# Kernel optimization log

Hardware: AMD Instinct MI355X
Metric: run time of the kernel (lower is better)

The kernel has to match this reference:

```python
import jax, jax.numpy as jnp
import numpy as np

N, E = 50000, 500000
HID, H, D = 128, 8, 16
ED, EGD = 32, 64


def _ln(x, g, b):
    m = x.mean(-1, keepdims=True)
    v = ((x - m) ** 2).mean(-1, keepdims=True)
    return (x - m) / jnp.sqrt(v + 1e-5) * g + b


def _gelu(x):
    return jax.nn.gelu(x, approximate=False)  # torch nn.GELU default (erf)


def setup_inputs() -> dict:
    key = jax.random.key(0)
    ks = jax.random.split(key, 24)
    s = lambda k, shape, scale=0.05: jax.random.normal(k, shape, jnp.float32) * scale
    inp = {
        "x": jax.random.normal(ks[0], (N, HID), jnp.float32),
        "edge_attr": jax.random.normal(ks[1], (E, ED), jnp.float32),
        "gamma": jax.random.uniform(ks[2], (N, HID), jnp.float32),
        "beta": jax.random.normal(ks[3], (N, HID), jnp.float32) * 0.1,
        "Wq": s(ks[4], (HID, H * D)),
        "Wk": s(ks[5], (HID, H * D)),
        "Wv": s(ks[6], (HID, H * D)),
        "Wo": s(ks[7], (H * D, HID)),
        "bo": jnp.zeros((HID,), jnp.float32),
        "ea_w1": s(ks[8], (ED, EGD)), "ea_b1": jnp.zeros((EGD,), jnp.float32),
        "ea_w2": s(ks[9], (EGD, H)), "ea_b2": jnp.zeros((H,), jnp.float32),
        "eg_w1": s(ks[10], (ED, EGD)), "eg_b1": jnp.zeros((EGD,), jnp.float32),
        "eg_w2": s(ks[11], (EGD, H * D)), "eg_b2": jnp.zeros((H * D,), jnp.float32),
        "ln1_g": jnp.ones((HID,), jnp.float32), "ln1_b": jnp.zeros((HID,), jnp.float32),
        "ln2_g": jnp.ones((HID,), jnp.float32), "ln2_b": jnp.zeros((HID,), jnp.float32),
        "ffn_w1": s(ks[12], (HID, 2 * HID)), "ffn_b1": jnp.zeros((2 * HID,), jnp.float32),
        "ffn_w2": s(ks[13], (2 * HID, HID)), "ffn_b2": jnp.zeros((HID,), jnp.float32),
        "edge_index": jax.random.randint(ks[14], (2, E), 0, N, jnp.int32),
    }
    return inp


def reference(x, edge_attr, gamma, beta, Wq, Wk, Wv, Wo, bo,
              ea_w1, ea_b1, ea_w2, ea_b2, eg_w1, eg_b1, eg_w2, eg_b2,
              ln1_g, ln1_b, ln2_g, ln2_b, ffn_w1, ffn_b1, ffn_w2, ffn_b2,
              edge_index):
    n = x.shape[0]
    src, dst = edge_index[0], edge_index[1]
    xn = _ln(x, ln1_g, ln1_b)
    Q = (xn @ Wq).reshape(n, H, D)
    K = (xn @ Wk).reshape(n, H, D)
    V = (xn @ Wv).reshape(n, H, D)
    # per-edge attention logits [E, H]
    logits = (Q[dst] * K[src]).sum(-1) * (D ** -0.5)
    logits = logits + (_gelu(edge_attr @ ea_w1 + ea_b1) @ ea_w2 + ea_b2)
    # sparse softmax over edges sharing a destination; torch version
    # initializes max buffer to zeros (include_self), so clamp max at 0
    m = jnp.maximum(jax.ops.segment_max(logits, dst, num_segments=n), 0.0)
    ex = jnp.exp(logits - m[dst])
    ssum = jax.ops.segment_sum(ex, dst, num_segments=n)
    attn = ex / (ssum[dst] + 1e-10)
    gate = jax.nn.sigmoid(_gelu(edge_attr @ eg_w1 + eg_b1) @ eg_w2 + eg_b2).reshape(-1, H, D)
    weighted = attn[..., None] * (gate * V[src])  # [E, H, D]
    agg = jax.ops.segment_sum(weighted, dst, num_segments=n).reshape(n, H * D)
    out = agg @ Wo + bo
    out = gamma * out + beta
    x = x + out
    x2 = _ln(x, ln2_g, ln2_b)
    f = _gelu(x2 @ ffn_w1 + ffn_b1) @ ffn_w2 + ffn_b2
    return x + f
```

## Files before the change

kernel.cpp:

```cpp
#include <hip/hip_runtime.h>

constexpr int N   = 50000;
constexpr int E   = 500000;
constexpr int HID = 128;
constexpr int NH  = 8;
constexpr int ED  = 32;
constexpr int EGD = 64;
constexpr int NB  = (N + 255) / 256;

typedef short  bf16x8 __attribute__((ext_vector_type(8)));
typedef float  f32x4  __attribute__((ext_vector_type(4)));

__device__ __forceinline__ float gelu_f(float v) {
    float u = v * v;
    float a = v * fmaf(u, -0.07135481283f, -1.5957691216f);
    float e = __expf(a);
    return v * __builtin_amdgcn_rcpf(1.f + e);
}
__device__ __forceinline__ float sigm_f(float v) {
    float e = __expf(-v);
    return __builtin_amdgcn_rcpf(1.f + e);
}
__device__ __forceinline__ unsigned short f2bf(float f) {
    return __builtin_bit_cast(unsigned short, static_cast<__bf16>(f));
}
__device__ __forceinline__ unsigned int pk2bf(float lo, float hi) {
    return (unsigned int)f2bf(lo) | ((unsigned int)f2bf(hi) << 16);
}
__device__ __forceinline__ float dot2(unsigned int a, unsigned int b) {
    float al = __uint_as_float(a << 16), ah = __uint_as_float(a & 0xffff0000u);
    float bl = __uint_as_float(b << 16), bh = __uint_as_float(b & 0xffff0000u);
    return al * bl + ah * bh;
}

__global__ __launch_bounds__(256) void k_cvt(
    const float* __restrict__ Wq, const float* __restrict__ Wk,
    const float* __restrict__ Wv, const float* __restrict__ Wo,
    const float* __restrict__ fw1, const float* __restrict__ fw2,
    const float* __restrict__ ea_w1, const float* __restrict__ ea_w2,
    const float* __restrict__ eg_w1, const float* __restrict__ eg_w2,
    unsigned short* __restrict__ dst)
{
    int f = blockIdx.x * 256 + threadIdx.x;
    if (f >= 18048) return;
    const float* W; int KT, srcN, base;
    if      (f < 2048)  { W = Wq;    KT = 4; srcN = 128; base = 0; }
    else if (f < 4096)  { W = Wk;    KT = 4; srcN = 128; base = 2048; }
    else if (f < 6144)  { W = Wv;    KT = 4; srcN = 128; base = 4096; }
    else if (f < 8192)  { W = Wo;    KT = 4; srcN = 128; base = 6144; }
    else if (f < 12288) { W = fw1;   KT = 4; srcN = 256; base = 8192; }
    else if (f < 16384) { W = fw2;   KT = 8; srcN = 128; base = 12288; }
    else if (f < 16640) { W = ea_w1; KT = 1; srcN = 64;  base = 16384; }
    else if (f < 16768) { W = ea_w2; KT = 2; srcN = 8;   base = 16640; }
    else if (f < 17024) { W = eg_w1; KT = 1; srcN = 64;  base = 16768; }
    else                { W = eg_w2; KT = 2; srcN = 128; base = 17024; }
    int fl = f - base, lane = fl & 63, t = fl >> 6;
    int ks = t % KT, nt = t / KT;
    int n  = nt * 16 + (lane & 15);
    int k0 = ks * 32 + (lane >> 4) * 8;
    union { unsigned short u[8]; uint4 v; } o;
#pragma unroll
    for (int j = 0; j < 8; j++)
        o.u[j] = (n < srcN) ? f2bf(W[(size_t)(k0 + j) * srcN + n]) : (unsigned short)0;
    *(uint4*)(dst + (size_t)f * 8) = o.v;
}

__global__ __launch_bounds__(256) void k_ln_qkv_mfma(
    const float* __restrict__ x, const float* __restrict__ g1, const float* __restrict__ b1,
    const unsigned short* __restrict__ wqkv,
    unsigned short* __restrict__ Q, unsigned short* __restrict__ K, unsigned short* __restrict__ V)
{
    __shared__ unsigned short xn_lds[16 * 128];
    const int tid = threadIdx.x;
    const int nodeBase = blockIdx.x * 16;

    {
        int nl = tid >> 4, q = tid & 15;
        const float4* xp = (const float4*)(x + (size_t)(nodeBase + nl) * HID + q * 8);
        float4 t0 = xp[0], t1 = xp[1];
        float v[8] = {t0.x, t0.y, t0.z, t0.w, t1.x, t1.y, t1.z, t1.w};
        float s = 0.f, ss = 0.f;
#pragma unroll
        for (int i = 0; i < 8; i++) { s += v[i]; ss += v[i] * v[i]; }
        s += __shfl_xor(s, 1); ss += __shfl_xor(ss, 1);
        s += __shfl_xor(s, 2); ss += __shfl_xor(ss, 2);
        s += __shfl_xor(s, 4); ss += __shfl_xor(ss, 4);
        s += __shfl_xor(s, 8); ss += __shfl_xor(ss, 8);
        float mean = s * (1.f / HID);
        float ri = rsqrtf(ss * (1.f / HID) - mean * mean + 1e-5f);
        union { unsigned short u[8]; uint4 v4; } o;
#pragma unroll
        for (int c = 0; c < 8; c++) {
            int col = q * 8 + c;
            o.u[c] = f2bf((v[c] - mean) * ri * g1[col] + b1[col]);
        }
        *(uint4*)&xn_lds[nl * 128 + (q ^ nl) * 8] = o.v4;
    }
    __syncthreads();

    const int wv = tid >> 6, lane = tid & 63;
    const int lm = lane & 15, kb = lane >> 4, rowq = kb * 4;
    bf16x8 af[4];
#pragma unroll
    for (int ks = 0; ks < 4; ks++)
        af[ks] = *(const bf16x8*)&xn_lds[lm * 128 + ((ks * 4 + kb) ^ lm) * 8];

    const int node = nodeBase + lm;
#pragma unroll
    for (int u = 0; u < 6; u++) {
        int nt = 6 * wv + u;
        f32x4 c = {0.f, 0.f, 0.f, 0.f};
#pragma unroll
        for (int ks = 0; ks < 4; ks++)
            c = __builtin_amdgcn_mfma_f32_16x16x32_bf16(
                    *(const bf16x8*)&wqkv[((size_t)(nt * 4 + ks) * 64 + lane) * 8],
                    af[ks], c, 0, 0, 0);
        unsigned short* O = (nt < 8) ? Q : ((nt < 16) ? K : V);
        uint2 o = make_uint2(pk2bf(c[0], c[1]), pk2bf(c[2], c[3]));
        *(uint2*)(O + (size_t)node * HID + (nt & 7) * 16 + rowq) = o;
    }
}

__global__ __launch_bounds__(256) void k_hist(const int* __restrict__ ei, int* __restrict__ cnt) {
    int e = blockIdx.x * 256 + threadIdx.x;
    if (e < E) atomicAdd(&cnt[ei[E + e]], 1);
}

__global__ __launch_bounds__(256) void k_bsum(const int* __restrict__ cnt, int* __restrict__ bsum) {
    int i = blockIdx.x * 256 + threadIdx.x;
    int v = (i < N) ? cnt[i] : 0;
#pragma unroll
    for (int m = 1; m < 64; m <<= 1) v += __shfl_xor(v, m);
    __shared__ int ws4[4];
    if ((threadIdx.x & 63) == 0) ws4[threadIdx.x >> 6] = v;
    __syncthreads();
    if (threadIdx.x == 0) bsum[blockIdx.x] = ws4[0] + ws4[1] + ws4[2] + ws4[3];
}

__global__ __launch_bounds__(256) void k_scan_b(const int* __restrict__ bsum, int* __restrict__ boff) {
    __shared__ int s[256];
    int t = threadIdx.x;
    int v = (t < NB) ? bsum[t] : 0;
    s[t] = v; __syncthreads();
    for (int off = 1; off < 256; off <<= 1) {
        int add = (t >= off) ? s[t - off] : 0;
        __syncthreads();
        s[t] += add;
        __syncthreads();
    }
    if (t < NB) boff[t] = s[t] - v;
}

__global__ __launch_bounds__(256) void k_scan_final(
    const int* __restrict__ cnt, const int* __restrict__ boff,
    int* __restrict__ starts, int* __restrict__ cursor)
{
    __shared__ int s[256];
    int t = threadIdx.x, i = blockIdx.x * 256 + t;
    int v = (i < N) ? cnt[i] : 0;
    s[t] = v; __syncthreads();
    for (int off = 1; off < 256; off <<= 1) {
        int add = (t >= off) ? s[t - off] : 0;
        __syncthreads();
        s[t] += add;
        __syncthreads();
    }
    int ex = boff[blockIdx.x] + s[t] - v;
    if (i < N) {
        starts[i] = ex;
        cursor[i] = ex;
        if (i == N - 1) starts[N] = ex + v;
    }
}

__global__ __launch_bounds__(256) void k_scatter(
    const int* __restrict__ ei, int* __restrict__ cursor, uint4* __restrict__ esd)
{
    int e = blockIdx.x * 256 + threadIdx.x;
    if (e < E) {
        int src = ei[e], dst = ei[E + e];
        int p = atomicAdd(&cursor[dst], 1);
        esd[p] = make_uint4((unsigned)src, (unsigned)dst, (unsigned)e, 0u);
    }
}

__global__ __launch_bounds__(256) void k_edge(
    const float* __restrict__ edge_attr, const uint4* __restrict__ esd,
    const unsigned short* __restrict__ Qb, const unsigned short* __restrict__ Kb,
    const unsigned short* __restrict__ Vb,
    const unsigned short* __restrict__ w1ea, const float* __restrict__ b1ea,
    const unsigned short* __restrict__ w2ea, const float* __restrict__ b2ea,
    const unsigned short* __restrict__ w1eg, const float* __restrict__ b1eg,
    const unsigned short* __restrict__ w2eg, const float* __restrict__ b2eg,
    float* __restrict__ logit_s, unsigned int* __restrict__ gv)
{
    __shared__ unsigned short ea_lds[256 * 32];
    __shared__ unsigned short sc_lds[4 * 16 * 64];
    __shared__ int perm_lds[256];
    __shared__ int src_lds[256];
    float* st16 = (float*)ea_lds;

    const int tid   = threadIdx.x;
    const int jBase = blockIdx.x * 256;
    const int lane  = tid & 63;
    const int wv    = tid >> 6;
    const int wBase = wv * 64;
    const int lm    = lane & 15;
    const int kb    = lane >> 4;
    const int rowq  = kb * 4;

    const int j  = jBase + tid;
    const int jj = (j < E) ? j : E - 1;
    const uint4 r4 = esd[jj];
    {
        perm_lds[tid] = (int)r4.z;
        src_lds[tid]  = (int)r4.x;
    }
    __syncthreads();

#pragma unroll
    for (int it = 0; it < 8; it++) {
        int idx = it * 256 + tid;
        int el = idx >> 3, c = (idx & 7) * 4;
        int ge = perm_lds[el];
        float4 v = *(const float4*)(edge_attr + (size_t)ge * ED + c);
        int g = ((c >> 3) ^ (el & 3));
        *(uint2*)&ea_lds[el * 32 + g * 8 + (c & 7)] =
            make_uint2(pk2bf(v.x, v.y), pk2bf(v.z, v.w));
    }
    __syncthreads();

    unsigned short* sc = &sc_lds[wv * 1024];

#pragma unroll 1
    for (int et = 0; et < 4; et++) {
        const int am = wBase + et * 16 + lm;
        const bf16x8 a1 = *(const bf16x8*)&ea_lds[am * 32 + (kb ^ (am & 3)) * 8];

        {
            f32x4 acc[4];
#pragma unroll
            for (int nt = 0; nt < 4; nt++) {
                f32x4 z = {0.f, 0.f, 0.f, 0.f};
                acc[nt] = __builtin_amdgcn_mfma_f32_16x16x32_bf16(
                    a1, *(const bf16x8*)&w1ea[(nt * 64 + lane) * 8], z, 0, 0, 0);
            }
#pragma unroll
            for (int nt = 0; nt < 4; nt++) {
                float bias = b1ea[nt * 16 + lm];
#pragma unroll
                for (int r = 0; r < 4; r++) {
                    int el = rowq + r;
                    int kg = nt * 2 + (lm >> 3);
                    sc[el * 64 + ((kg ^ (el & 7)) * 8) + (lm & 7)] =
                        f2bf(gelu_f(acc[nt][r] + bias));
                }
            }
        }
        {
            bf16x8 f0 = *(const bf16x8*)&sc[lm * 64 + ((kb ^ (lm & 7)) * 8)];
            bf16x8 f1 = *(const bf16x8*)&sc[lm * 64 + (((4 + kb) ^ (lm & 7)) * 8)];
            float bias = b2ea[lm & 7];
            f32x4 acc = {bias, bias, bias, bias};
            acc = __builtin_amdgcn_mfma_f32_16x16x32_bf16(
                f0, *(const bf16x8*)&w2ea[(0 * 64 + lane) * 8], acc, 0, 0, 0);
            acc = __builtin_amdgcn_mfma_f32_16x16x32_bf16(
                f1, *(const bf16x8*)&w2ea[(1 * 64 + lane) * 8], acc, 0, 0, 0);
            if (lm < 8) {
#pragma unroll
                for (int r = 0; r < 4; r++)
                    st16[(wBase + et * 16 + rowq + r) * 16 + lm] = acc[r];
            }
        }
        {
            f32x4 acc[4];
#pragma unroll
            for (int nt = 0; nt < 4; nt++) {
                f32x4 z = {0.f, 0.f, 0.f, 0.f};
                acc[nt] = __builtin_amdgcn_mfma_f32_16x16x32_bf16(
                    a1, *(const bf16x8*)&w1eg[(nt * 64 + lane) * 8], z, 0, 0, 0);
            }
#pragma unroll
            for (int nt = 0; nt < 4; nt++) {
                float bias = b1eg[nt * 16 + lm];
#pragma unroll
                for (int r = 0; r < 4; r++) {
                    int el = rowq + r;
                    int kg = nt * 2 + (lm >> 3);
                    sc[el * 64 + ((kg ^ (el & 7)) * 8) + (lm & 7)] =
                        f2bf(gelu_f(acc[nt][r] + bias));
                }
            }
        }
        {
            bf16x8 h0 = *(const bf16x8*)&sc[lm * 64 + ((kb ^ (lm & 7)) * 8)];
            bf16x8 h1 = *(const bf16x8*)&sc[lm * 64 + (((4 + kb) ^ (lm & 7)) * 8)];
            const int e   = jBase + wBase + et * 16 + lm;
            const int src = src_lds[wBase + et * 16 + lm];
            const unsigned short* vrow = Vb + (size_t)src * HID;
            const bool ok = (e < E);
            unsigned int* gvo = gv + (size_t)e * 64 + kb * 2;
#pragma unroll
            for (int mt = 0; mt < 8; mt++) {
                float4 b4 = *(const float4*)&b2eg[mt * 16 + rowq];
                f32x4 acc = {b4.x, b4.y, b4.z, b4.w};
                acc = __builtin_amdgcn_mfma_f32_16x16x32_bf16(
                    *(const bf16x8*)&w2eg[((mt * 2 + 0) * 64 + lane) * 8], h0, acc, 0, 0, 0);
                acc = __builtin_amdgcn_mfma_f32_16x16x32_bf16(
                    *(const bf16x8*)&w2eg[((mt * 2 + 1) * 64 + lane) * 8], h1, acc, 0, 0, 0);
                uint2 vv = *(const uint2*)(vrow + mt * 16 + rowq);
                float w0 = sigm_f(acc[0]) * __uint_as_float(vv.x << 16);
                float w1 = sigm_f(acc[1]) * __uint_as_float(vv.x & 0xffff0000u);
                float w2 = sigm_f(acc[2]) * __uint_as_float(vv.y << 16);
                float w3 = sigm_f(acc[3]) * __uint_as_float(vv.y & 0xffff0000u);
                uint2 o = make_uint2(pk2bf(w0, w1), pk2bf(w2, w3));
                if (ok) *(uint2*)(gvo + mt * 8) = o;
            }
        }
    }

    {
        if (j < E) {
            int src = (int)r4.x, dst = (int)r4.y;
            const uint4* qp = (const uint4*)(Qb + (size_t)dst * HID);
            const uint4* kp = (const uint4*)(Kb + (size_t)src * HID);
            float lg[8];
#pragma unroll
            for (int h = 0; h < 8; h++) {
                float dot = 0.f;
#pragma unroll
                for (int t = 0; t < 2; t++) {
                    uint4 q = qp[h * 2 + t], k4 = kp[h * 2 + t];
                    dot += dot2(q.x, k4.x) + dot2(q.y, k4.y) + dot2(q.z, k4.z) + dot2(q.w, k4.w);
                }
                lg[h] = __expf(fminf(st16[tid * 16 + h] + 0.25f * dot, 80.f));
            }
            float4* op = (float4*)(logit_s + (size_t)j * NH);
            op[0] = make_float4(lg[0], lg[1], lg[2], lg[3]);
            op[1] = make_float4(lg[4], lg[5], lg[6], lg[7]);
        }
    }
}

__global__ __launch_bounds__(256) void k_agg2(
    const int* __restrict__ starts, const unsigned int* __restrict__ gv,
    const float* __restrict__ logit_s, float* __restrict__ agg)
{
    int wave = threadIdx.x >> 6, lane = threadIdx.x & 63;
    int dst = blockIdx.x * 4 + wave;
    if (dst >= N) return;
    int s0 = starts[dst], s1 = starts[dst + 1];
    int head = lane >> 3;
    float ssum = 0.f, ax = 0.f, ay = 0.f;
#pragma unroll 4
    for (int j = s0; j < s1; j++) {
        float e = logit_s[(size_t)j * NH + head];
        unsigned int u = gv[(size_t)j * 64 + lane];
        ssum += e;
        ax += e * __uint_as_float(u << 16);
        ay += e * __uint_as_float(u & 0xffff0000u);
    }
    float rs = __builtin_amdgcn_rcpf(ssum + 1e-10f);
    float2* o = (float2*)(agg + (size_t)dst * HID + lane * 2);
    *o = make_float2(ax * rs, ay * rs);
}

__global__ __launch_bounds__(256) void k_node_out_mfma(
    const float* __restrict__ x, const float* __restrict__ gamma, const float* __restrict__ beta,
    const unsigned short* __restrict__ wo_f, const float* __restrict__ bo,
    const float* __restrict__ g2, const float* __restrict__ b2,
    const unsigned short* __restrict__ fw1_f, const float* __restrict__ fb1,
    const unsigned short* __restrict__ fw2_f, const float* __restrict__ fb2,
    const float* __restrict__ agg, float* __restrict__ out)
{
    __shared__ unsigned short a_lds[16 * 128];
    __shared__ unsigned short f1_lds[16 * 256];
    __shared__ float2 sums_lds[16][4];
    const int tid = threadIdx.x;
    const int nodeBase = blockIdx.x * 16;

    {
        int nl = tid >> 4, q = tid & 15;
        const float4* ap = (const float4*)(agg + (size_t)(nodeBase + nl) * HID + q * 8);
        float4 t0 = ap[0], t1 = ap[1];
        uint4 o = make_uint4(pk2bf(t0.x, t0.y), pk2bf(t0.z, t0.w),
                             pk2bf(t1.x, t1.y), pk2bf(t1.z, t1.w));
        *(uint4*)&a_lds[nl * 128 + (q ^ nl) * 8] = o;
    }
    __syncthreads();

    const int wv = tid >> 6, lane = tid & 63;
    const int lm = lane & 15, kb = lane >> 4, rowq = kb * 4;

    f32x4 xo[2];
    {
        bf16x8 af[4];
#pragma unroll
        for (int ks = 0; ks < 4; ks++)
            af[ks] = *(const bf16x8*)&a_lds[lm * 128 + ((ks * 4 + kb) ^ lm) * 8];
#pragma unroll
        for (int t = 0; t < 2; t++) {
            int nt = 2 * wv + t;
            f32x4 c = {0.f, 0.f, 0.f, 0.f};
#pragma unroll
            for (int ks = 0; ks < 4; ks++)
                c = __builtin_amdgcn_mfma_f32_16x16x32_bf16(
                        af[ks], *(const bf16x8*)&wo_f[((size_t)(nt * 4 + ks) * 64 + lane) * 8],
                        c, 0, 0, 0);
            xo[t] = c;
        }
    }

    float x1v[2][4];
#pragma unroll
    for (int t = 0; t < 2; t++) {
        int col = (2 * wv + t) * 16 + lm;
        float boc = bo[col];
#pragma unroll
        for (int r = 0; r < 4; r++) {
            size_t idx = (size_t)(nodeBase + rowq + r) * HID + col;
            x1v[t][r] = x[idx] + gamma[idx] * (xo[t][r] + boc) + beta[idx];
        }
    }

    {
        float s2[4], q2[4];
#pragma unroll
        for (int r = 0; r < 4; r++) {
            s2[r] = x1v[0][r] + x1v[1][r];
            q2[r] = x1v[0][r] * x1v[0][r] + x1v[1][r] * x1v[1][r];
        }
#pragma unroll
        for (int m = 1; m < 16; m <<= 1)
#pragma unroll
            for (int r = 0; r < 4; r++) { s2[r] += __shfl_xor(s2[r], m); q2[r] += __shfl_xor(q2[r], m); }
        if (lm == 0) {
#pragma unroll
            for (int r = 0; r < 4; r++)
                sums_lds[rowq + r][wv] = make_float2(s2[r], q2[r]);
        }
    }
    __syncthreads();
    float mu4[4], ri4[4];
#pragma unroll
    for (int r = 0; r < 4; r++) {
        float2 p0 = sums_lds[rowq + r][0], p1 = sums_lds[rowq + r][1];
        float2 p2 = sums_lds[rowq + r][2], p3 = sums_lds[rowq + r][3];
        float s = p0.x + p1.x + p2.x + p3.x;
        float q = p0.y + p1.y + p2.y + p3.y;
        float mu = s * (1.f / HID);
        mu4[r] = mu;
        ri4[r] = rsqrtf(q * (1.f / HID) - mu * mu + 1e-5f);
    }

#pragma unroll
    for (int t = 0; t < 2; t++) {
        int col = (2 * wv + t) * 16 + lm;
        float g2c = g2[col], b2c = b2[col];
#pragma unroll
        for (int r = 0; r < 4; r++) {
            float xn = (x1v[t][r] - mu4[r]) * ri4[r] * g2c + b2c;
            int row = rowq + r;
            int g = col >> 3;
            a_lds[row * 128 + (g ^ row) * 8 + (col & 7)] = f2bf(xn);
        }
    }
    __syncthreads();

    {
        bf16x8 af[4];
#pragma unroll
        for (int ks = 0; ks < 4; ks++)
            af[ks] = *(const bf16x8*)&a_lds[lm * 128 + ((ks * 4 + kb) ^ lm) * 8];
#pragma unroll
        for (int u = 0; u < 4; u++) {
            int nt = 4 * wv + u;
            f32x4 c = {0.f, 0.f, 0.f, 0.f};
#pragma unroll
            for (int ks = 0; ks < 4; ks++)
                c = __builtin_amdgcn_mfma_f32_16x16x32_bf16(
                        af[ks], *(const bf16x8*)&fw1_f[((size_t)(nt * 4 + ks) * 64 + lane) * 8],
                        c, 0, 0, 0);
            int col = nt * 16 + lm;
            float fbc = fb1[col];
#pragma unroll
            for (int r = 0; r < 4; r++) {
                int row = rowq + r;
                int g = col >> 3;
                int phys = (g & 16) | ((g ^ row) & 15);
                f1_lds[row * 256 + phys * 8 + (col & 7)] = f2bf(gelu_f(c[r] + fbc));
            }
        }
    }
    __syncthreads();

    {
        bf16x8 af[8];
#pragma unroll
        for (int ks = 0; ks < 8; ks++) {
            int g = ks * 4 + kb;
            int phys = (g & 16) | ((g ^ lm) & 15);
            af[ks] = *(const bf16x8*)&f1_lds[lm * 256 + phys * 8];
        }
#pragma unroll
        for (int t = 0; t < 2; t++) {
            int nt = 2 * wv + t;
            f32x4 c = {0.f, 0.f, 0.f, 0.f};
#pragma unroll
            for (int ks = 0; ks < 8; ks++)
                c = __builtin_amdgcn_mfma_f32_16x16x32_bf16(
                        af[ks], *(const bf16x8*)&fw2_f[((size_t)(nt * 8 + ks) * 64 + lane) * 8],
                        c, 0, 0, 0);
            int col = nt * 16 + lm;
            float fbc = fb2[col];
#pragma unroll
            for (int r = 0; r < 4; r++) {
                int node = nodeBase + rowq + r;
                out[(size_t)node * HID + col] = x1v[t][r] + c[r] + fbc;
            }
        }
    }
}

extern "C" void kernel_launch(void* const* d_in, const int* in_sizes, int n_in,
                              void* d_out, int out_size, void* d_ws, size_t ws_size,
                              hipStream_t stream)
{
    const float* x         = (const float*)d_in[0];
    const float* edge_attr = (const float*)d_in[1];
    const float* gamma     = (const float*)d_in[2];
    const float* beta      = (const float*)d_in[3];
    const float* Wq        = (const float*)d_in[4];
    const float* Wk        = (const float*)d_in[5];
    const float* Wv        = (const float*)d_in[6];
    const float* Wo        = (const float*)d_in[7];
    const float* bo        = (const float*)d_in[8];
    const float* ea_w1     = (const float*)d_in[9];
    const float* ea_b1     = (const float*)d_in[10];
    const float* ea_w2     = (const float*)d_in[11];
    const float* ea_b2     = (const float*)d_in[12];
    const float* eg_w1     = (const float*)d_in[13];
    const float* eg_b1     = (const float*)d_in[14];
    const float* eg_w2     = (const float*)d_in[15];
    const float* eg_b2     = (const float*)d_in[16];
    const float* ln1_g     = (const float*)d_in[17];
    const float* ln1_b     = (const float*)d_in[18];
    const float* ln2_g     = (const float*)d_in[19];
    const float* ln2_b     = (const float*)d_in[20];
    const float* fw1       = (const float*)d_in[21];
    const float* fb1       = (const float*)d_in[22];
    const float* fw2       = (const float*)d_in[23];
    const float* fb2       = (const float*)d_in[24];
    const int*   ei        = (const int*)d_in[25];

    char* wsb = (char*)d_ws;
    size_t off = 0;
    auto alloc = [&](size_t bytes) { void* p = wsb + off; off += (bytes + 255) & ~(size_t)255; return p; };

    unsigned short* Qb = (unsigned short*)alloc((size_t)N * HID * 2);
    unsigned short* Kb = (unsigned short*)alloc((size_t)N * HID * 2);
    unsigned short* Vb = (unsigned short*)alloc((size_t)N * HID * 2);
    float* logit_s = (float*)alloc((size_t)E * NH * 4);
    float* aggb    = (float*)alloc((size_t)N * HID * 4);
    int*   cnt     = (int*)alloc((size_t)N * 4);
    int*   starts  = (int*)alloc((size_t)(N + 1) * 4);
    int*   cursor  = (int*)alloc((size_t)N * 4);
    int*   bsum    = (int*)alloc((size_t)NB * 4);
    int*   boff    = (int*)alloc((size_t)NB * 4);
    uint4* esd     = (uint4*)alloc((size_t)E * 16);
    unsigned int*   gvb   = (unsigned int*)alloc((size_t)E * 64 * 4);
    unsigned short* fragW = (unsigned short*)alloc((size_t)18048 * 8 * 2);
    float* outp = (float*)d_out;

    unsigned short* wqkv_f = fragW;
    unsigned short* wo_f   = fragW + (size_t)6144  * 8;
    unsigned short* fw1_f  = fragW + (size_t)8192  * 8;
    unsigned short* fw2_f  = fragW + (size_t)12288 * 8;
    unsigned short* w1ea_f = fragW + (size_t)16384 * 8;
    unsigned short* w2ea_f = fragW + (size_t)16640 * 8;
    unsigned short* w1eg_f = fragW + (size_t)16768 * 8;
    unsigned short* w2eg_f = fragW + (size_t)17024 * 8;

    hipMemsetAsync(cnt, 0, (size_t)N * sizeof(int), stream);

    const int EB = (E + 255) / 256;
    const int NBLK16 = (N + 15) / 16;
    k_cvt<<<(18048 + 255) / 256, 256, 0, stream>>>(Wq, Wk, Wv, Wo, fw1, fw2,
                                                   ea_w1, ea_w2, eg_w1, eg_w2, fragW);
    k_ln_qkv_mfma<<<NBLK16, 256, 0, stream>>>(x, ln1_g, ln1_b, wqkv_f, Qb, Kb, Vb);
    k_hist<<<EB, 256, 0, stream>>>(ei, cnt);
    k_bsum<<<NB, 256, 0, stream>>>(cnt, bsum);
    k_scan_b<<<1, 256, 0, stream>>>(bsum, boff);
    k_scan_final<<<NB, 256, 0, stream>>>(cnt, boff, starts, cursor);
    k_scatter<<<EB, 256, 0, stream>>>(ei, cursor, esd);
    k_edge<<<EB, 256, 0, stream>>>(edge_attr, esd, Qb, Kb, Vb,
                                   w1ea_f, ea_b1, w2ea_f, ea_b2,
                                   w1eg_f, eg_b1, w2eg_f, eg_b2,
                                   logit_s, gvb);
    k_agg2<<<(N + 3) / 4, 256, 0, stream>>>(starts, gvb, logit_s, aggb);
    k_node_out_mfma<<<NBLK16, 256, 0, stream>>>(x, gamma, beta, wo_f, bo, ln2_g, ln2_b,
                                                fw1_f, fb1, fw2_f, fb2, aggb, outp);
}
```

Measured before the change: 446.1 us.

## Fuse preprocessing kernels and fold edge aggregation into node output kernel

```diff
diff --git a/kernel.cpp b/kernel.cpp
--- a/kernel.cpp
+++ b/kernel.cpp
@@ -7,6 +7,8 @@
 constexpr int ED  = 32;
 constexpr int EGD = 64;
 constexpr int NB  = (N + 255) / 256;
+constexpr int EB  = (E + 255) / 256;
+constexpr int NBLK16 = (N + 15) / 16;
 
 typedef short  bf16x8 __attribute__((ext_vector_type(8)));
 typedef float  f32x4  __attribute__((ext_vector_type(4)));
@@ -33,7 +35,8 @@
     return al * bl + ah * bh;
 }
 
-__global__ __launch_bounds__(256) void k_cvt(
+__global__ __launch_bounds__(256) void k_hist_cvt(
+    const int* __restrict__ ei, int* __restrict__ cnt,
     const float* __restrict__ Wq, const float* __restrict__ Wk,
     const float* __restrict__ Wv, const float* __restrict__ Wo,
     const float* __restrict__ fw1, const float* __restrict__ fw2,
@@ -41,7 +44,12 @@
     const float* __restrict__ eg_w1, const float* __restrict__ eg_w2,
     unsigned short* __restrict__ dst)
 {
-    int f = blockIdx.x * 256 + threadIdx.x;
+    if (blockIdx.x < EB) {
+        int e = blockIdx.x * 256 + threadIdx.x;
+        if (e < E) atomicAdd(&cnt[ei[E + e]], 1);
+        return;
+    }
+    int f = (blockIdx.x - EB) * 256 + threadIdx.x;
     if (f >= 18048) return;
     const float* W; int KT, srcN, base;
     if      (f < 2048)  { W = Wq;    KT = 4; srcN = 128; base = 0; }
@@ -65,13 +73,28 @@
     *(uint4*)(dst + (size_t)f * 8) = o.v;
 }
 
-__global__ __launch_bounds__(256) void k_ln_qkv_mfma(
+__global__ __launch_bounds__(256) void k_lnqkv_bsum(
     const float* __restrict__ x, const float* __restrict__ g1, const float* __restrict__ b1,
     const unsigned short* __restrict__ wqkv,
-    unsigned short* __restrict__ Q, unsigned short* __restrict__ K, unsigned short* __restrict__ V)
+    unsigned short* __restrict__ Q, unsigned short* __restrict__ K, unsigned short* __restrict__ V,
+    const int* __restrict__ cnt, int* __restrict__ bsum)
 {
     __shared__ unsigned short xn_lds[16 * 128];
     const int tid = threadIdx.x;
+
+    if (blockIdx.x >= NBLK16) {
+        int bb = blockIdx.x - NBLK16;
+        int i = bb * 256 + tid;
+        int v = (i < N) ? cnt[i] : 0;
+#pragma unroll
+        for (int m = 1; m < 64; m <<= 1) v += __shfl_xor(v, m);
+        int* ws4 = (int*)xn_lds;
+        if ((tid & 63) == 0) ws4[tid >> 6] = v;
+        __syncthreads();
+        if (tid == 0) bsum[bb] = ws4[0] + ws4[1] + ws4[2] + ws4[3];
+        return;
+    }
+
     const int nodeBase = blockIdx.x * 16;
 
     {
@@ -121,42 +144,22 @@
     }
 }
 
-__global__ __launch_bounds__(256) void k_hist(const int* __restrict__ ei, int* __restrict__ cnt) {
-    int e = blockIdx.x * 256 + threadIdx.x;
-    if (e < E) atomicAdd(&cnt[ei[E + e]], 1);
-}
-
-__global__ __launch_bounds__(256) void k_bsum(const int* __restrict__ cnt, int* __restrict__ bsum) {
-    int i = blockIdx.x * 256 + threadIdx.x;
-    int v = (i < N) ? cnt[i] : 0;
-#pragma unroll
-    for (int m = 1; m < 64; m <<= 1) v += __shfl_xor(v, m);
+__global__ __launch_bounds__(256) void k_scan_final2(
+    const int* __restrict__ cnt, const int* __restrict__ bsum,
+    int* __restrict__ starts, int* __restrict__ cursor)
+{
+    __shared__ int s[256];
     __shared__ int ws4[4];
-    if ((threadIdx.x & 63) == 0) ws4[threadIdx.x >> 6] = v;
-    __syncthreads();
-    if (threadIdx.x == 0) bsum[blockIdx.x] = ws4[0] + ws4[1] + ws4[2] + ws4[3];
-}
-
-__global__ __launch_bounds__(256) void k_scan_b(const int* __restrict__ bsum, int* __restrict__ boff) {
-    __shared__ int s[256];
-    int t = threadIdx.x;
-    int v = (t < NB) ? bsum[t] : 0;
-    s[t] = v; __syncthreads();
-    for (int off = 1; off < 256; off <<= 1) {
-        int add = (t >= off) ? s[t - off] : 0;
-        __syncthreads();
-        s[t] += add;
-        __syncthreads();
-    }
-    if (t < NB) boff[t] = s[t] - v;
-}
-
-__global__ __launch_bounds__(256) void k_scan_final(
-    const int* __restrict__ cnt, const int* __restrict__ boff,
-    int* __restrict__ starts, int* __restrict__ cursor)
-{
-    __shared__ int s[256];
-    int t = threadIdx.x, i = blockIdx.x * 256 + t;
+    const int t = threadIdx.x, b = blockIdx.x;
+
+    int pv = (t < b) ? bsum[t] : 0;
+#pragma unroll
+    for (int m = 1; m < 64; m <<= 1) pv += __shfl_xor(pv, m);
+    if ((t & 63) == 0) ws4[t >> 6] = pv;
+    __syncthreads();
+    const int pre = ws4[0] + ws4[1] + ws4[2] + ws4[3];
+
+    int i = b * 256 + t;
     int v = (i < N) ? cnt[i] : 0;
     s[t] = v; __syncthreads();
     for (int off = 1; off < 256; off <<= 1) {
@@ -165,7 +168,7 @@
         s[t] += add;
         __syncthreads();
     }
-    int ex = boff[blockIdx.x] + s[t] - v;
+    int ex = pre + s[t] - v;
     if (i < N) {
         starts[i] = ex;
         cursor[i] = ex;
@@ -342,36 +345,14 @@
     }
 }
 
-__global__ __launch_bounds__(256) void k_agg2(
-    const int* __restrict__ starts, const unsigned int* __restrict__ gv,
-    const float* __restrict__ logit_s, float* __restrict__ agg)
-{
-    int wave = threadIdx.x >> 6, lane = threadIdx.x & 63;
-    int dst = blockIdx.x * 4 + wave;
-    if (dst >= N) return;
-    int s0 = starts[dst], s1 = starts[dst + 1];
-    int head = lane >> 3;
-    float ssum = 0.f, ax = 0.f, ay = 0.f;
-#pragma unroll 4
-    for (int j = s0; j < s1; j++) {
-        float e = logit_s[(size_t)j * NH + head];
-        unsigned int u = gv[(size_t)j * 64 + lane];
-        ssum += e;
-        ax += e * __uint_as_float(u << 16);
-        ay += e * __uint_as_float(u & 0xffff0000u);
-    }
-    float rs = __builtin_amdgcn_rcpf(ssum + 1e-10f);
-    float2* o = (float2*)(agg + (size_t)dst * HID + lane * 2);
-    *o = make_float2(ax * rs, ay * rs);
-}
-
 __global__ __launch_bounds__(256) void k_node_out_mfma(
     const float* __restrict__ x, const float* __restrict__ gamma, const float* __restrict__ beta,
     const unsigned short* __restrict__ wo_f, const float* __restrict__ bo,
     const float* __restrict__ g2, const float* __restrict__ b2,
     const unsigned short* __restrict__ fw1_f, const float* __restrict__ fb1,
     const unsigned short* __restrict__ fw2_f, const float* __restrict__ fb2,
-    const float* __restrict__ agg, float* __restrict__ out)
+    const int* __restrict__ starts, const unsigned int* __restrict__ gv,
+    const float* __restrict__ logit_s, float* __restrict__ out)
 {
     __shared__ unsigned short a_lds[16 * 128];
     __shared__ unsigned short f1_lds[16 * 256];
@@ -379,18 +360,30 @@
     const int tid = threadIdx.x;
     const int nodeBase = blockIdx.x * 16;
 
-    {
-        int nl = tid >> 4, q = tid & 15;
-        const float4* ap = (const float4*)(agg + (size_t)(nodeBase + nl) * HID + q * 8);
-        float4 t0 = ap[0], t1 = ap[1];
-        uint4 o = make_uint4(pk2bf(t0.x, t0.y), pk2bf(t0.z, t0.w),
-                             pk2bf(t1.x, t1.y), pk2bf(t1.z, t1.w));
-        *(uint4*)&a_lds[nl * 128 + (q ^ nl) * 8] = o;
-    }
-    __syncthreads();
-
     const int wv = tid >> 6, lane = tid & 63;
     const int lm = lane & 15, kb = lane >> 4, rowq = kb * 4;
+
+#pragma unroll 1
+    for (int i = 0; i < 4; i++) {
+        const int nl = wv * 4 + i;
+        const int dst = nodeBase + nl;
+        const int s0 = starts[dst], s1 = starts[dst + 1];
+        const int head = lane >> 3;
+        float ssum = 0.f, ax = 0.f, ay = 0.f;
+#pragma unroll 4
+        for (int jj = s0; jj < s1; jj++) {
+            float e = logit_s[(size_t)jj * NH + head];
+            unsigned int u = gv[(size_t)jj * 64 + lane];
+            ssum += e;
+            ax += e * __uint_as_float(u << 16);
+            ay += e * __uint_as_float(u & 0xffff0000u);
+        }
+        float rs = __builtin_amdgcn_rcpf(ssum + 1e-10f);
+        int g = lane >> 2;
+        *(unsigned int*)&a_lds[nl * 128 + ((g ^ nl) * 8) + ((2 * lane) & 7)] =
+            pk2bf(ax * rs, ay * rs);
+    }
+    __syncthreads();
 
     f32x4 xo[2];
     {
@@ -561,12 +554,10 @@
     unsigned short* Kb = (unsigned short*)alloc((size_t)N * HID * 2);
     unsigned short* Vb = (unsigned short*)alloc((size_t)N * HID * 2);
     float* logit_s = (float*)alloc((size_t)E * NH * 4);
-    float* aggb    = (float*)alloc((size_t)N * HID * 4);
     int*   cnt     = (int*)alloc((size_t)N * 4);
     int*   starts  = (int*)alloc((size_t)(N + 1) * 4);
     int*   cursor  = (int*)alloc((size_t)N * 4);
     int*   bsum    = (int*)alloc((size_t)NB * 4);
-    int*   boff    = (int*)alloc((size_t)NB * 4);
     uint4* esd     = (uint4*)alloc((size_t)E * 16);
     unsigned int*   gvb   = (unsigned int*)alloc((size_t)E * 64 * 4);
     unsigned short* fragW = (unsigned short*)alloc((size_t)18048 * 8 * 2);
@@ -583,21 +574,17 @@
 
     hipMemsetAsync(cnt, 0, (size_t)N * sizeof(int), stream);
 
-    const int EB = (E + 255) / 256;
-    const int NBLK16 = (N + 15) / 16;
-    k_cvt<<<(18048 + 255) / 256, 256, 0, stream>>>(Wq, Wk, Wv, Wo, fw1, fw2,
-                                                   ea_w1, ea_w2, eg_w1, eg_w2, fragW);
-    k_ln_qkv_mfma<<<NBLK16, 256, 0, stream>>>(x, ln1_g, ln1_b, wqkv_f, Qb, Kb, Vb);
-    k_hist<<<EB, 256, 0, stream>>>(ei, cnt);
-    k_bsum<<<NB, 256, 0, stream>>>(cnt, bsum);
-    k_scan_b<<<1, 256, 0, stream>>>(bsum, boff);
-    k_scan_final<<<NB, 256, 0, stream>>>(cnt, boff, starts, cursor);
+    k_hist_cvt<<<EB + (18048 + 255) / 256, 256, 0, stream>>>(
+        ei, cnt, Wq, Wk, Wv, Wo, fw1, fw2, ea_w1, ea_w2, eg_w1, eg_w2, fragW);
+    k_lnqkv_bsum<<<NBLK16 + NB, 256, 0, stream>>>(
+        x, ln1_g, ln1_b, wqkv_f, Qb, Kb, Vb, cnt, bsum);
+    k_scan_final2<<<NB, 256, 0, stream>>>(cnt, bsum, starts, cursor);
     k_scatter<<<EB, 256, 0, stream>>>(ei, cursor, esd);
     k_edge<<<EB, 256, 0, stream>>>(edge_attr, esd, Qb, Kb, Vb,
                                    w1ea_f, ea_b1, w2ea_f, ea_b2,
                                    w1eg_f, eg_b1, w2eg_f, eg_b2,
                                    logit_s, gvb);
-    k_agg2<<<(N + 3) / 4, 256, 0, stream>>>(starts, gvb, logit_s, aggb);
     k_node_out_mfma<<<NBLK16, 256, 0, stream>>>(x, gamma, beta, wo_f, bo, ln2_g, ln2_b,
-                                                fw1_f, fb1, fw2_f, fb2, aggb, outp);
-}
+                                                fw1_f, fb1, fw2_f, fb2,
+                                                starts, gvb, logit_s, outp);
+}
```

Result: no change. 450.2 us (+0.9%).
